# Kernel optimization log

Hardware: AMD Instinct MI355X
Metric: run time of the kernel (lower is better)

## Reference

```python
import jax, jax.numpy as jnp
import numpy as np

B, S, H = 8, 8192, 1024
CAPACITY_FACTOR = 0.5


def setup_inputs() -> dict:
    key = jax.random.key(0)
    ks = jax.random.split(key, 5)
    sc = lambda fan: np.float32(1.0 / np.sqrt(fan))
    return {
        "x": jax.random.normal(ks[0], (B, S, H), dtype=jnp.float32),
        # router: Linear(H, H//4) -> ReLU -> Linear(H//4, 1)
        "W1": jax.random.normal(ks[1], (H, H // 4), dtype=jnp.float32) * sc(H),
        "b1": jnp.zeros((H // 4,), dtype=jnp.float32),
        "W2": jax.random.normal(ks[2], (H // 4, 1), dtype=jnp.float32) * sc(H // 4),
        "b2": jnp.zeros((1,), dtype=jnp.float32),
        # external layer_fn realized as a dense layer: gelu(x @ Wl)
        "Wl": jax.random.normal(ks[3], (H, H), dtype=jnp.float32) * sc(H),
    }


def reference(x, W1, b1, W2, b2, Wl):
    # router scores [B, S, 1]
    scores = jax.nn.relu(jnp.einsum("bsh,hd->bsd", x, W1) + b1)
    scores = jnp.einsum("bsd,do->bso", scores, W2) + b2
    routing_weights = jax.nn.sigmoid(scores)  # [B, S, 1]

    # eval path: process only top-capacity tokens per batch row
    capacity = int(S * CAPACITY_FACTOR)
    _, top_idx = jax.lax.top_k(scores[..., 0], capacity)  # [B, C]

    selected = jnp.take_along_axis(x, top_idx[..., None], axis=1)  # [B, C, H]
    processed = jax.nn.gelu(jnp.einsum("bch,hd->bcd", selected, Wl))  # layer_fn

    batch_idx = jnp.arange(x.shape[0])[:, None]  # [B, 1]
    output = x.at[batch_idx, top_idx].set(processed)  # scatter back into clone of x
    return output, routing_weights
```

## Files before the change

### kernel.cpp

```cpp
#include <hip/hip_runtime.h>
#include <stdint.h>

#define B_   8
#define S_   8192
#define H_   1024
#define HQ_  256
#define CAP_ 4096
#define UCAP_ (S_-CAP_)
#define M_   (B_*CAP_)
#define EPSB 0.012f
#define LCAP 8192

using f32x4 = __attribute__((ext_vector_type(4))) float;
using s16x8 = __attribute__((ext_vector_type(8))) short;

__device__ __forceinline__ unsigned short f2bf(float f) {
  unsigned u = __float_as_uint(f);
  u += 0x7FFF + ((u >> 16) & 1);
  return (unsigned short)(u >> 16);
}
__device__ __forceinline__ float bf2f(unsigned short h) {
  return __uint_as_float(((unsigned)h) << 16);
}

__device__ __forceinline__ float gelu_f(float v) {
  float s = v + 0.044715f * v * v * v;
  float e = __expf(-1.5957691216057308f * s);
  return v * __builtin_amdgcn_rcpf(1.0f + e);
}

__device__ __forceinline__ unsigned mono(float f) {
  unsigned u = __float_as_uint(f);
  return (u & 0x80000000u) ? ~u : (u | 0x80000000u);
}
__device__ __forceinline__ float unmono(unsigned k) {
  unsigned u = (k & 0x80000000u) ? (k & 0x7fffffffu) : ~k;
  return __uint_as_float(u);
}

__device__ __forceinline__ void gload_lds16(const void* g, void* l) {
  __builtin_amdgcn_global_load_lds(
      (const __attribute__((address_space(1))) void*)(uintptr_t)g,
      (__attribute__((address_space(3))) void*)(uintptr_t)l,
      16, 0, 0);
}

__device__ __forceinline__ float radix_select_T(
    const float* __restrict__ srow, unsigned* hist,
    unsigned* sh_b, unsigned* sh_gt, int tid) {
  unsigned prefix = 0; int plen = 0; unsigned rank = CAP_;
  #pragma unroll
  for (int round = 0; round < 3; ++round) {
    const int nb = (round < 2) ? 11 : 10;
    hist[tid] = 0; hist[tid + 1024] = 0;
    __syncthreads();
    for (int i = tid; i < S_; i += 1024) {
      unsigned k = mono(srow[i]);
      if (plen == 0 || (k >> (32 - plen)) == prefix) {
        unsigned bucket = (k << plen) >> (32 - nb);
        atomicAdd(&hist[bucket], 1u);
      }
    }
    __syncthreads();
    for (int s = 1; s < 2048; s <<= 1) {
      unsigned t0 = (tid + s < 2048) ? hist[tid + s] : 0;
      unsigned t1 = (tid + 1024 + s < 2048) ? hist[tid + 1024 + s] : 0;
      __syncthreads();
      hist[tid] += t0; hist[tid + 1024] += t1;
      __syncthreads();
    }
    #pragma unroll
    for (int h = 0; h < 2; ++h) {
      int i = tid + h * 1024;
      unsigned ge = hist[i];
      unsigned gt = (i < 2047) ? hist[i + 1] : 0;
      if (gt < rank && rank <= ge) { *sh_b = (unsigned)i; *sh_gt = gt; }
    }
    __syncthreads();
    prefix = (prefix << nb) | *sh_b;
    plen += nb;
    rank -= *sh_gt;
    __syncthreads();
  }
  return unmono(prefix);
}

__global__ __launch_bounds__(256) void prep_kernel(
    const float* __restrict__ W1, unsigned short* __restrict__ w1t_hi,
    const float* __restrict__ wl, unsigned short* __restrict__ wlt) {
  __shared__ float tile[32][33];
  const int bid = blockIdx.x;
  const int tx = threadIdx.x, ty = threadIdx.y;
  if (bid < 256) {
    int n0 = (bid & 7) * 32, k0 = (bid >> 3) * 32;
    for (int i = ty; i < 32; i += 8) tile[i][tx] = W1[(size_t)(k0 + i) * HQ_ + n0 + tx];
    __syncthreads();
    for (int i = ty; i < 32; i += 8)
      w1t_hi[(size_t)(n0 + i) * H_ + k0 + tx] = f2bf(tile[tx][i]);
  } else {
    int idx = bid - 256;
    int x0 = (idx & 31) * 32, y0 = (idx >> 5) * 32;
    for (int i = ty; i < 32; i += 8) tile[i][tx] = wl[(size_t)(y0 + i) * H_ + x0 + tx];
    __syncthreads();
    for (int i = ty; i < 32; i += 8)
      wlt[(size_t)(x0 + i) * H_ + y0 + tx] = f2bf(tile[tx][i]);
  }
}

#define RIA(U, KT, BUF) do {                                                   \
    int c_i = (U) * 512 + t;                                                   \
    int row_ = c_i >> 4, q_ = c_i & 15;                                        \
    int qz_ = q_ ^ (row_ & 15);                                                \
    gload_lds16(x + (size_t)(m0 + row_) * H_ + (KT) * 64 + qz_ * 4,            \
                &Af[BUF][(size_t)c_i * 4]);                                    \
  } while (0)
#define RIB(U, KT, BUF) do {                                                   \
    int row_ = (U) * 64 + (t >> 3);                                            \
    int sl_ = t & 7;                                                           \
    int slz_ = sl_ ^ (row_ & 7);                                               \
    gload_lds16(w1t_hi + (size_t)row_ * H_ + (KT) * 64 + slz_ * 8,             \
                &Bs[BUF][(size_t)row_ * 64 + sl_ * 8]);                        \
  } while (0)
#define RPH(P, ISSUE, WAITCODE) do {                                           \
    s16x8 af[2];                                                               \
    _Pragma("unroll")                                                          \
    for (int kk = 0; kk < 2; ++kk) {                                           \
      int r_ = wr * 64 + (P) * 16 + r16;                                       \
      int g2 = 2 * (kk * 4 + ks);                                              \
      float4 f0 = *(const float4*)&Af[c_][((size_t)r_ * 16 + (g2 ^ (r_ & 15))) * 4];       \
      float4 f1 = *(const float4*)&Af[c_][((size_t)r_ * 16 + ((g2 + 1) ^ (r_ & 15))) * 4]; \
      unsigned short hh[8];                                                    \
      hh[0] = f2bf(f0.x); hh[1] = f2bf(f0.y); hh[2] = f2bf(f0.z); hh[3] = f2bf(f0.w); \
      hh[4] = f2bf(f1.x); hh[5] = f2bf(f1.y); hh[6] = f2bf(f1.z); hh[7] = f2bf(f1.w); \
      af[kk] = *(s16x8*)hh;                                                    \
    }                                                                          \
    if ((P) == 0) {                                                            \
      _Pragma("unroll")                                                        \
      for (int j = 0; j < 4; ++j)                                              \
        _Pragma("unroll")                                                      \
        for (int kk = 0; kk < 2; ++kk) {                                       \
          int r_ = wc * 64 + j * 16 + r16;                                     \
          bfr[j][kk] = *(const s16x8*)&Bs[c_][(size_t)r_ * 64 + ((kk * 4 + ks) ^ (r_ & 7)) * 8]; \
        }                                                                      \
    }                                                                          \
    ISSUE                                                                      \
    __builtin_amdgcn_s_barrier();                                              \
    asm volatile("s_waitcnt lgkmcnt(0)" ::: "memory");                         \
    __builtin_amdgcn_sched_barrier(0);                                         \
    __builtin_amdgcn_s_setprio(1);                                             \
    _Pragma("unroll")                                                          \
    for (int j = 0; j < 4; ++j)                                                \
      _Pragma("unroll")                                                        \
      for (int kk = 0; kk < 2; ++kk)                                           \
        acc[P][j] = __builtin_amdgcn_mfma_f32_16x16x32_bf16(                   \
            af[kk], bfr[j][kk], acc[P][j], 0, 0, 0);                           \
    __builtin_amdgcn_s_setprio(0);                                             \
    __builtin_amdgcn_sched_barrier(0);                                         \
    WAITCODE                                                                   \
    __builtin_amdgcn_s_barrier();                                              \
    __builtin_amdgcn_sched_barrier(0);                                         \
  } while (0)

__global__ __launch_bounds__(512, 1) void router_mfma_kernel(
    const float* __restrict__ x, const unsigned short* __restrict__ w1t_hi,
    const float* __restrict__ b1, const float* __restrict__ W2,
    const float* __restrict__ b2, float* __restrict__ scores,
    float* __restrict__ rw, int* __restrict__ count) {
  __shared__ __align__(16) float Af[2][128 * 64];
  __shared__ __align__(16) unsigned short Bs[2][256 * 64];
  __shared__ float part[128][4];
  const int t = threadIdx.x;
  const int lane = t & 63, w = t >> 6;
  const int m0 = blockIdx.x * 128;
  if (blockIdx.x == 0 && t == 0) *count = 0;
  const int wr = w >> 2, wc = w & 3;
  const int r16 = lane & 15, ks = lane >> 4;

  f32x4 acc[4][4];
  #pragma unroll
  for (int i = 0; i < 4; ++i)
    #pragma unroll
    for (int j = 0; j < 4; ++j) acc[i][j] = (f32x4){0.f, 0.f, 0.f, 0.f};

  RIB(0, 0, 0); RIB(1, 0, 0); RIB(2, 0, 0); RIB(3, 0, 0);
  RIA(0, 0, 0); RIA(2, 0, 0); RIA(1, 0, 0); RIA(3, 0, 0);
  asm volatile("s_waitcnt vmcnt(2)" ::: "memory");
  __syncthreads();

  for (int kt = 0; kt < 15; ++kt) {
    const int c_ = kt & 1, nb_ = c_ ^ 1;
    const int kn = kt + 1;
    s16x8 bfr[4][2];
    RPH(0, { RIB(0, kn, nb_); RIB(1, kn, nb_); }, {});
    RPH(1, { RIB(2, kn, nb_); RIB(3, kn, nb_); },
        { asm volatile("s_waitcnt vmcnt(4)" ::: "memory"); });
    RPH(2, { RIA(0, kn, nb_); RIA(2, kn, nb_); }, {});
    RPH(3, { RIA(1, kn, nb_); RIA(3, kn, nb_); },
        { asm volatile("s_waitcnt vmcnt(2)" ::: "memory"); });
  }
  {
    const int c_ = 1;
    s16x8 bfr[4][2];
    RPH(0, {;}, {});
    RPH(1, {;}, { asm volatile("s_waitcnt vmcnt(0)" ::: "memory"); });
    RPH(2, {;}, {});
    RPH(3, {;}, {});
  }

  float b1v[4], w2v[4];
  #pragma unroll
  for (int j = 0; j < 4; ++j) {
    int n = wc * 64 + j * 16 + r16;
    b1v[j] = b1[n]; w2v[j] = W2[n];
  }
  const int g4 = lane >> 4;
  #pragma unroll
  for (int i = 0; i < 4; ++i) {
    #pragma unroll
    for (int r = 0; r < 4; ++r) {
      float p = 0.f;
      #pragma unroll
      for (int j = 0; j < 4; ++j) {
        float h = acc[i][j][r] + b1v[j];
        h = fmaxf(h, 0.f);
        p = fmaf(h, w2v[j], p);
      }
      p += __shfl_xor(p, 1);
      p += __shfl_xor(p, 2);
      p += __shfl_xor(p, 4);
      p += __shfl_xor(p, 8);
      if (r16 == 0) part[wr * 64 + i * 16 + g4 * 4 + r][wc] = p;
    }
  }
  __syncthreads();
  if (t < 128) {
    float sc = part[t][0] + part[t][1] + part[t][2] + part[t][3] + b2[0];
    scores[m0 + t] = sc;
    rw[m0 + t] = 1.f / (1.f + expf(-sc));
  }
}

__global__ __launch_bounds__(1024) void select_band_kernel(
    const float* __restrict__ scores, int* __restrict__ list,
    int* __restrict__ count) {
  __shared__ unsigned hist[2048];
  __shared__ unsigned sh_b, sh_gt;
  const int b = blockIdx.x;
  const int tid = threadIdx.x;
  const float* srow = scores + (size_t)b * S_;
  const float T = radix_select_T(srow, hist, &sh_b, &sh_gt, tid);
  for (int i = tid; i < S_; i += 1024) {
    float s = srow[i];
    if (fabsf(s - T) <= EPSB) {
      int p = atomicAdd(count, 1);
      if (p < LCAP) list[p] = b * S_ + i;
    }
  }
}

__global__ __launch_bounds__(256) void recompute_kernel(
    const float* __restrict__ x, const float* __restrict__ W1,
    const float* __restrict__ b1, const float* __restrict__ W2,
    const float* __restrict__ b2, const int* __restrict__ list,
    const int* __restrict__ count, float* __restrict__ scores,
    float* __restrict__ rw) {
  __shared__ float xr[4][H_];
  __shared__ float red[4][4];
  int n = *count; if (n > LCAP) n = LCAP;
  const int j = threadIdx.x;
  for (int base = blockIdx.x * 4; base < n; base += gridDim.x * 4) {
    int nt = n - base; if (nt > 4) nt = 4;
    for (int tt = 0; tt < 4; ++tt) {
      int tok = list[base + ((tt < nt) ? tt : 0)];
      const float* xrow = x + (size_t)tok * H_;
      for (int k = j; k < H_; k += 256) xr[tt][k] = xrow[k];
    }
    __syncthreads();
    float a0 = 0.f, a1 = 0.f, a2 = 0.f, a3 = 0.f;
    for (int k = 0; k < H_; ++k) {
      float wv = W1[(size_t)k * HQ_ + j];
      a0 = fmaf(xr[0][k], wv, a0);
      a1 = fmaf(xr[1][k], wv, a1);
      a2 = fmaf(xr[2][k], wv, a2);
      a3 = fmaf(xr[3][k], wv, a3);
    }
    float aa[4] = {a0, a1, a2, a3};
    #pragma unroll
    for (int tt = 0; tt < 4; ++tt) {
      float h = fmaxf(aa[tt] + b1[j], 0.f);
      float v = h * W2[j];
      v += __shfl_xor(v, 1);  v += __shfl_xor(v, 2);  v += __shfl_xor(v, 4);
      v += __shfl_xor(v, 8);  v += __shfl_xor(v, 16); v += __shfl_xor(v, 32);
      if ((j & 63) == 0) red[tt][j >> 6] = v;
    }
    __syncthreads();
    if (j < nt) {
      int tok = list[base + j];
      float sc = red[j][0] + red[j][1] + red[j][2] + red[j][3] + b2[0];
      scores[tok] = sc;
      rw[tok] = 1.f / (1.f + expf(-sc));
    }
    __syncthreads();
  }
}

__global__ __launch_bounds__(1024) void compact_kernel(
    const float* __restrict__ scores, int* __restrict__ comp,
    int* __restrict__ ucomp) {
  __shared__ unsigned hist[2048];
  __shared__ unsigned sh_b, sh_gt;
  __shared__ int wc_eq[16], wc_sel[16], red[16];
  const int b = blockIdx.x;
  const float* srow = scores + (size_t)b * S_;
  const int tid = threadIdx.x, lane = tid & 63, wid = tid >> 6;
  const float T = radix_select_T(srow, hist, &sh_b, &sh_gt, tid);

  int cgt = 0;
  #pragma unroll
  for (int c = 0; c < 8; ++c) cgt += (srow[c * 1024 + tid] > T) ? 1 : 0;
  cgt += __shfl_xor(cgt, 1);  cgt += __shfl_xor(cgt, 2);  cgt += __shfl_xor(cgt, 4);
  cgt += __shfl_xor(cgt, 8);  cgt += __shfl_xor(cgt, 16); cgt += __shfl_xor(cgt, 32);
  if (lane == 0) red[wid] = cgt;
  __syncthreads();
  int cnt_gt = 0;
  #pragma unroll
  for (int i = 0; i < 16; ++i) cnt_gt += red[i];
  const int need = CAP_ - cnt_gt;

  int* crow = comp + b * CAP_;
  int* urow = ucomp + b * UCAP_;
  int sel_base = 0, unsel_base = 0, eq_base = 0;
  __syncthreads();
  for (int c = 0; c < 8; ++c) {
    int idx = c * 1024 + tid;
    float s = srow[idx];
    bool gt = s > T, eq = (s == T);
    unsigned long long meq = __ballot(eq);
    if (lane == 0) wc_eq[wid] = __popcll(meq);
    __syncthreads();
    int eq_off = eq_base, eq_tot = 0;
    #pragma unroll
    for (int w2 = 0; w2 < 16; ++w2) { if (w2 < wid) eq_off += wc_eq[w2]; eq_tot += wc_eq[w2]; }
    int eqpos = eq_off + __popcll(meq & ((1ull << lane) - 1));
    bool take = gt || (eq && eqpos < need);
    unsigned long long mt = __ballot(take);
    if (lane == 0) wc_sel[wid] = __popcll(mt);
    __syncthreads();
    int sel_off = sel_base, sel_tot = 0;
    #pragma unroll
    for (int w2 = 0; w2 < 16; ++w2) { if (w2 < wid) sel_off += wc_sel[w2]; sel_tot += wc_sel[w2]; }
    if (take) {
      crow[sel_off + __popcll(mt & ((1ull << lane) - 1))] = idx;
    } else {
      int un_off = unsel_base + wid * 64 - (sel_off - sel_base);
      urow[un_off + __popcll(~mt & ((1ull << lane) - 1))] = idx;
    }
    sel_base += sel_tot; unsel_base += 1024 - sel_tot; eq_base += eq_tot;
    __syncthreads();
  }
}

__global__ __launch_bounds__(256) void gather_copy_kernel(
    const float* __restrict__ x, const int* __restrict__ comp,
    const int* __restrict__ ucomp, unsigned short* __restrict__ xg,
    float* __restrict__ out) {
  const int bid = blockIdx.x;
  const int tx = threadIdx.x;
  if (bid < M_) {
    int b = bid >> 12, cc = bid & (CAP_ - 1);
    int token = comp[b * CAP_ + cc];
    float4 v = ((const float4*)(x + ((size_t)(b * S_ + token)) * H_))[tx];
    ushort4 o;
    o.x = f2bf(v.x); o.y = f2bf(v.y); o.z = f2bf(v.z); o.w = f2bf(v.w);
    *(ushort4*)&xg[(size_t)bid * H_ + tx * 4] = o;
  } else {
    int i = bid - M_;
    int b = i >> 12, r = i & (UCAP_ - 1);
    int token = ucomp[b * UCAP_ + r];
    size_t row = (size_t)b * S_ + token;
    ((float4*)(out + row * H_))[tx] = ((const float4*)(x + row * H_))[tx];
  }
}

#define ISSUE_A(P, KT, BUF) do {                                               \
    int row_ = half * 128 + (P) * 32 + rr;                                     \
    int slz_ = sl ^ (row_ & 7);                                                \
    gload_lds16(xg + (size_t)(m0 + row_) * H_ + (KT) * 64 + slz_ * 8,          \
                &As[BUF][row_ * 64 + sl * 8]);                                 \
  } while (0)
#define ISSUE_B(P, KT, BUF) do {                                               \
    int row_ = half * 128 + (P) * 32 + rr;                                     \
    int slz_ = sl ^ (row_ & 7);                                                \
    gload_lds16(wlt + (size_t)(n0 + row_) * H_ + (KT) * 64 + slz_ * 8,         \
                &Bs[BUF][row_ * 64 + sl * 8]);                                 \
  } while (0)
#define MOE_PHASE(P, ISSUE, WAITSTR) do {                                      \
    s16x8 af[2][2];                                                            \
    _Pragma("unroll")                                                          \
    for (int i = 0; i < 2; ++i)                                                \
      _Pragma("unroll")                                                        \
      for (int kk = 0; kk < 2; ++kk) {                                         \
        int r_ = wr * 128 + (2 * (P) + i) * 16 + r16;                          \
        af[i][kk] = *(const s16x8*)&As[c_][r_ * 64 + ((kk * 4 + ks) ^ (r_ & 7)) * 8]; \
      }                                                                        \
    if ((P) == 0) {                                                            \
      _Pragma("unroll")                                                        \
      for (int j = 0; j < 4; ++j)                                              \
        _Pragma("unroll")                                                      \
        for (int kk = 0; kk < 2; ++kk) {                                       \
          int r_ = wc * 64 + j * 16 + r16;                                     \
          bfr[j][kk] = *(const s16x8*)&Bs[c_][r_ * 64 + ((kk * 4 + ks) ^ (r_ & 7)) * 8]; \
        }                                                                      \
    }                                                                          \
    ISSUE                                                                      \
    __builtin_amdgcn_s_barrier();                                              \
    asm volatile("s_waitcnt lgkmcnt(0)" ::: "memory");                         \
    __builtin_amdgcn_sched_barrier(0);                                         \
    __builtin_amdgcn_s_setprio(1);                                             \
    _Pragma("unroll")                                                          \
    for (int i = 0; i < 2; ++i)                                                \
      _Pragma("unroll")                                                        \
      for (int j = 0; j < 4; ++j)                                              \
        _Pragma("unroll")                                                      \
        for (int kk = 0; kk < 2; ++kk)                                         \
          acc[2 * (P) + i][j] = __builtin_amdgcn_mfma_f32_16x16x32_bf16(       \
              af[i][kk], bfr[j][kk], acc[2 * (P) + i][j], 0, 0, 0);            \
    __builtin_amdgcn_s_setprio(0);                                             \
    __builtin_amdgcn_sched_barrier(0);                                         \
    asm volatile("s_waitcnt " WAITSTR ::: "memory");                           \
    __builtin_amdgcn_s_barrier();                                              \
    __builtin_amdgcn_sched_barrier(0);                                         \
  } while (0)

__global__ __launch_bounds__(512, 1) void moe_gemm_kernel(
    const unsigned short* __restrict__ xg, const unsigned short* __restrict__ wlt,
    const int* __restrict__ comp, float* __restrict__ out) {
  __shared__ __align__(16) unsigned short As[2][256 * 64];
  __shared__ __align__(16) unsigned short Bs[2][256 * 64];
  __shared__ int toks[256];
  const int t = threadIdx.x;
  const int lane = t & 63, w = t >> 6;
  const int bid = blockIdx.x;
  const int xcd = bid & 7, wb = bid >> 3;
  const int m0 = (xcd * 16 + (wb >> 2)) * 256;
  const int n0 = (wb & 3) * 256;
  const int bb = m0 >> 12;
  if (t < 256) toks[t] = comp[bb * CAP_ + (m0 & (CAP_ - 1)) + t];
  const int wr = w >> 2, wc = w & 3;
  const int r16 = lane & 15, ks = lane >> 4;
  const int half = t >> 8, rr = (t >> 3) & 31, sl = t & 7;

  f32x4 acc[8][4];
  #pragma unroll
  for (int i = 0; i < 8; ++i)
    #pragma unroll
    for (int j = 0; j < 4; ++j) acc[i][j] = (f32x4){0.f, 0.f, 0.f, 0.f};

  ISSUE_B(0, 0, 0); ISSUE_B(1, 0, 0); ISSUE_B(2, 0, 0); ISSUE_B(3, 0, 0);
  ISSUE_A(0, 0, 0); ISSUE_A(1, 0, 0); ISSUE_A(2, 0, 0); ISSUE_A(3, 0, 0);
  asm volatile("s_waitcnt vmcnt(3)" ::: "memory");
  __syncthreads();

  for (int kt = 0; kt < 15; ++kt) {
    const int c_ = kt & 1, nb_ = c_ ^ 1;
    const int kn = kt + 1;
    s16x8 bfr[4][2];
    MOE_PHASE(0, { ISSUE_B(0, kn, nb_); ISSUE_B(1, kn, nb_); }, "vmcnt(4)");
    MOE_PHASE(1, { ISSUE_B(2, kn, nb_); ISSUE_B(3, kn, nb_); }, "vmcnt(5)");
    MOE_PHASE(2, { ISSUE_A(0, kn, nb_); ISSUE_A(1, kn, nb_); }, "vmcnt(6)");
    MOE_PHASE(3, { ISSUE_A(2, kn, nb_); ISSUE_A(3, kn, nb_); }, "vmcnt(3)");
  }
  {
    const int c_ = 1;
    s16x8 bfr[4][2];
    MOE_PHASE(0, {;}, "vmcnt(2)");
    MOE_PHASE(1, {;}, "vmcnt(1)");
    MOE_PHASE(2, {;}, "vmcnt(0)");
    MOE_PHASE(3, {;}, "vmcnt(63)");
  }

  const int g4 = lane >> 4;
  #pragma unroll
  for (int i = 0; i < 8; ++i) {
    #pragma unroll
    for (int r = 0; r < 4; ++r) {
      int rl = wr * 128 + i * 16 + g4 * 4 + r;
      int token = toks[rl];
      float* orow = out + ((size_t)(bb * S_ + token)) * H_ + n0 + wc * 64;
      #pragma unroll
      for (int j = 0; j < 4; ++j)
        orow[j * 16 + r16] = gelu_f(acc[i][j][r]);
    }
  }
}

extern "C" void kernel_launch(void* const* d_in, const int* in_sizes, int n_in,
                              void* d_out, int out_size, void* d_ws, size_t ws_size,
                              hipStream_t stream) {
  const float* x  = (const float*)d_in[0];
  const float* W1 = (const float*)d_in[1];
  const float* b1 = (const float*)d_in[2];
  const float* W2 = (const float*)d_in[3];
  const float* b2 = (const float*)d_in[4];
  const float* Wl = (const float*)d_in[5];
  float* out = (float*)d_out;
  float* rw  = out + (size_t)B_ * S_ * H_;

  char* ws = (char*)d_ws;
  float* scores        = (float*)ws;
  int*   comp          = (int*)(ws + (256 << 10));
  int*   count         = (int*)(ws + (384 << 10) + 256);
  int*   list          = (int*)(ws + (384 << 10) + 512);
  int*   ucomp         = (int*)(ws + (448 << 10));
  unsigned short* wlt  = (unsigned short*)(ws + (1 << 20));
  unsigned short* xg   = (unsigned short*)(ws + (3 << 20));
  unsigned short* w1t_hi = xg;

  hipLaunchKernelGGL(prep_kernel, dim3(1280), dim3(32, 8), 0, stream,
                     W1, w1t_hi, Wl, wlt);
  hipLaunchKernelGGL(router_mfma_kernel, dim3((B_*S_)/128), dim3(512), 0, stream,
                     x, w1t_hi, b1, W2, b2, scores, rw, count);
  hipLaunchKernelGGL(select_band_kernel, dim3(B_), dim3(1024), 0, stream,
                     scores, list, count);
  hipLaunchKernelGGL(recompute_kernel, dim3(128), dim3(256), 0, stream,
                     x, W1, b1, W2, b2, list, count, scores, rw);
  hipLaunchKernelGGL(compact_kernel, dim3(B_), dim3(1024), 0, stream,
                     scores, comp, ucomp);
  hipLaunchKernelGGL(gather_copy_kernel, dim3(M_ + B_*UCAP_), dim3(256), 0, stream,
                     x, comp, ucomp, xg, out);
  hipLaunchKernelGGL(moe_gemm_kernel, dim3((M_/256)*(H_/256)), dim3(512), 0, stream,
                     xg, wlt, comp, out);
}
```

Measured before the change: 390.2 us.

## Shrink MoE GEMM tile to 128x128 with four waves and two-phase pipeline

New measurement: 418.3 us. 7.2% more time.

```diff
diff --git a/kernel.cpp b/kernel.cpp
--- a/kernel.cpp
+++ b/kernel.cpp
@@ -382,25 +382,27 @@
   }
 }
 
-#define ISSUE_A(P, KT, BUF) do {                                               \
-    int row_ = half * 128 + (P) * 32 + rr;                                     \
-    int slz_ = sl ^ (row_ & 7);                                                \
+#define MISSUE_A(U, KT, BUF) do {                                              \
+    int c_i = (U) * 256 + t;                                                   \
+    int row_ = c_i >> 3, sl_ = c_i & 7;                                        \
+    int slz_ = sl_ ^ (row_ & 7);                                               \
     gload_lds16(xg + (size_t)(m0 + row_) * H_ + (KT) * 64 + slz_ * 8,          \
-                &As[BUF][row_ * 64 + sl * 8]);                                 \
+                &As[BUF][c_i * 8]);                                            \
   } while (0)
-#define ISSUE_B(P, KT, BUF) do {                                               \
-    int row_ = half * 128 + (P) * 32 + rr;                                     \
-    int slz_ = sl ^ (row_ & 7);                                                \
+#define MISSUE_B(U, KT, BUF) do {                                              \
+    int c_i = (U) * 256 + t;                                                   \
+    int row_ = c_i >> 3, sl_ = c_i & 7;                                        \
+    int slz_ = sl_ ^ (row_ & 7);                                               \
     gload_lds16(wlt + (size_t)(n0 + row_) * H_ + (KT) * 64 + slz_ * 8,         \
-                &Bs[BUF][row_ * 64 + sl * 8]);                                 \
+                &Bs[BUF][c_i * 8]);                                            \
   } while (0)
-#define MOE_PHASE(P, ISSUE, WAITSTR) do {                                      \
+#define MPH(P, ISSUE, WAITCODE) do {                                           \
     s16x8 af[2][2];                                                            \
     _Pragma("unroll")                                                          \
     for (int i = 0; i < 2; ++i)                                                \
       _Pragma("unroll")                                                        \
       for (int kk = 0; kk < 2; ++kk) {                                         \
-        int r_ = wr * 128 + (2 * (P) + i) * 16 + r16;                          \
+        int r_ = wr * 64 + ((P) * 2 + i) * 16 + r16;                           \
         af[i][kk] = *(const s16x8*)&As[c_][r_ * 64 + ((kk * 4 + ks) ^ (r_ & 7)) * 8]; \
       }                                                                        \
     if ((P) == 0) {                                                            \
@@ -423,68 +425,69 @@
       for (int j = 0; j < 4; ++j)                                              \
         _Pragma("unroll")                                                      \
         for (int kk = 0; kk < 2; ++kk)                                         \
-          acc[2 * (P) + i][j] = __builtin_amdgcn_mfma_f32_16x16x32_bf16(       \
-              af[i][kk], bfr[j][kk], acc[2 * (P) + i][j], 0, 0, 0);            \
+          acc[(P) * 2 + i][j] = __builtin_amdgcn_mfma_f32_16x16x32_bf16(       \
+              af[i][kk], bfr[j][kk], acc[(P) * 2 + i][j], 0, 0, 0);            \
     __builtin_amdgcn_s_setprio(0);                                             \
     __builtin_amdgcn_sched_barrier(0);                                         \
-    asm volatile("s_waitcnt " WAITSTR ::: "memory");                           \
+    WAITCODE                                                                   \
     __builtin_amdgcn_s_barrier();                                              \
     __builtin_amdgcn_sched_barrier(0);                                         \
   } while (0)
 
-__global__ __launch_bounds__(512, 1) void moe_gemm_kernel(
+__global__ __launch_bounds__(256) void moe_gemm_kernel(
     const unsigned short* __restrict__ xg, const unsigned short* __restrict__ wlt,
     const int* __restrict__ comp, float* __restrict__ out) {
-  __shared__ __align__(16) unsigned short As[2][256 * 64];
-  __shared__ __align__(16) unsigned short Bs[2][256 * 64];
-  __shared__ int toks[256];
+  __shared__ __align__(16) unsigned short As[2][128 * 64];
+  __shared__ __align__(16) unsigned short Bs[2][128 * 64];
+  __shared__ int toks[128];
   const int t = threadIdx.x;
   const int lane = t & 63, w = t >> 6;
   const int bid = blockIdx.x;
-  const int xcd = bid & 7, wb = bid >> 3;
-  const int m0 = (xcd * 16 + (wb >> 2)) * 256;
-  const int n0 = (wb & 3) * 256;
+  const int xcd = bid & 7, r_ = bid >> 3;
+  const int m0 = (xcd * 32 + (r_ >> 3)) * 128;
+  const int n0 = (r_ & 7) * 128;
   const int bb = m0 >> 12;
-  if (t < 256) toks[t] = comp[bb * CAP_ + (m0 & (CAP_ - 1)) + t];
-  const int wr = w >> 2, wc = w & 3;
+  if (t < 128) toks[t] = comp[bb * CAP_ + (m0 & (CAP_ - 1)) + t];
+  const int wr = w >> 1, wc = w & 1;
   const int r16 = lane & 15, ks = lane >> 4;
-  const int half = t >> 8, rr = (t >> 3) & 31, sl = t & 7;
-
-  f32x4 acc[8][4];
-  #pragma unroll
-  for (int i = 0; i < 8; ++i)
+
+  f32x4 acc[4][4];
+  #pragma unroll
+  for (int i = 0; i < 4; ++i)
     #pragma unroll
     for (int j = 0; j < 4; ++j) acc[i][j] = (f32x4){0.f, 0.f, 0.f, 0.f};
 
-  ISSUE_B(0, 0, 0); ISSUE_B(1, 0, 0); ISSUE_B(2, 0, 0); ISSUE_B(3, 0, 0);
-  ISSUE_A(0, 0, 0); ISSUE_A(1, 0, 0); ISSUE_A(2, 0, 0); ISSUE_A(3, 0, 0);
-  asm volatile("s_waitcnt vmcnt(3)" ::: "memory");
-  __syncthreads();
+  MISSUE_B(0, 0, 0); MISSUE_B(1, 0, 0); MISSUE_B(2, 0, 0); MISSUE_B(3, 0, 0);
+  MISSUE_A(0, 0, 0); MISSUE_A(2, 0, 0); MISSUE_A(1, 0, 0); MISSUE_A(3, 0, 0);
+  asm volatile("s_waitcnt vmcnt(2)" ::: "memory");
+  asm volatile("s_waitcnt lgkmcnt(0)" ::: "memory");
+  __builtin_amdgcn_s_barrier();
+  __builtin_amdgcn_sched_barrier(0);
 
   for (int kt = 0; kt < 15; ++kt) {
     const int c_ = kt & 1, nb_ = c_ ^ 1;
     const int kn = kt + 1;
     s16x8 bfr[4][2];
-    MOE_PHASE(0, { ISSUE_B(0, kn, nb_); ISSUE_B(1, kn, nb_); }, "vmcnt(4)");
-    MOE_PHASE(1, { ISSUE_B(2, kn, nb_); ISSUE_B(3, kn, nb_); }, "vmcnt(5)");
-    MOE_PHASE(2, { ISSUE_A(0, kn, nb_); ISSUE_A(1, kn, nb_); }, "vmcnt(6)");
-    MOE_PHASE(3, { ISSUE_A(2, kn, nb_); ISSUE_A(3, kn, nb_); }, "vmcnt(3)");
+    MPH(0, { MISSUE_B(0, kn, nb_); MISSUE_B(1, kn, nb_);
+             MISSUE_B(2, kn, nb_); MISSUE_B(3, kn, nb_); },
+        { asm volatile("s_waitcnt vmcnt(4)" ::: "memory"); });
+    MPH(1, { MISSUE_A(0, kn, nb_); MISSUE_A(2, kn, nb_);
+             MISSUE_A(1, kn, nb_); MISSUE_A(3, kn, nb_); },
+        { asm volatile("s_waitcnt vmcnt(2)" ::: "memory"); });
   }
   {
     const int c_ = 1;
     s16x8 bfr[4][2];
-    MOE_PHASE(0, {;}, "vmcnt(2)");
-    MOE_PHASE(1, {;}, "vmcnt(1)");
-    MOE_PHASE(2, {;}, "vmcnt(0)");
-    MOE_PHASE(3, {;}, "vmcnt(63)");
+    MPH(0, {;}, { asm volatile("s_waitcnt vmcnt(0)" ::: "memory"); });
+    MPH(1, {;}, {;});
   }
 
   const int g4 = lane >> 4;
   #pragma unroll
-  for (int i = 0; i < 8; ++i) {
+  for (int i = 0; i < 4; ++i) {
     #pragma unroll
     for (int r = 0; r < 4; ++r) {
-      int rl = wr * 128 + i * 16 + g4 * 4 + r;
+      int rl = wr * 64 + i * 16 + g4 * 4 + r;
       int token = toks[rl];
       float* orow = out + ((size_t)(bb * S_ + token)) * H_ + n0 + wc * 64;
       #pragma unroll
@@ -528,6 +531,6 @@
                      scores, comp, ucomp);
   hipLaunchKernelGGL(gather_copy_kernel, dim3(M_ + B_*UCAP_), dim3(256), 0, stream,
                      x, comp, ucomp, xg, out);
-  hipLaunchKernelGGL(moe_gemm_kernel, dim3((M_/256)*(H_/256)), dim3(512), 0, stream,
+  hipLaunchKernelGGL(moe_gemm_kernel, dim3((M_/128)*(H_/128)), dim3(256), 0, stream,
                      xg, wlt, comp, out);
 }
```
